# Kernel tuning notes

Hardware: AMD Instinct MI355X
Metric: run time of the kernel (lower is better)

## Reference

```python
import jax, jax.numpy as jnp
import numpy as np

NUM_RELATIONS = 16


def rgcn_conv(x, src, dst, etype, W, root, b):
    """PyG-style RGCNConv: per-relation mean aggregation + root weight + bias.

    x: [N, din]; W: [R, din, dout]; root: [din, dout]; b: [dout].
    """
    N, din = x.shape
    R = W.shape[0]
    E = src.shape[0]
    xe = x[src]                                   # [E, din] gather
    seg = etype * N + dst                          # combined (relation, dst) key
    sums = jax.ops.segment_sum(xe, seg, num_segments=R * N)        # [R*N, din]
    cnt = jax.ops.segment_sum(jnp.ones((E,), x.dtype), seg, num_segments=R * N)
    mean = (sums / jnp.maximum(cnt, 1.0)[:, None]).reshape(R, N, din)
    # mean-then-transform == PyG transform-then-mean (linearity)
    out = jnp.einsum('rnd,rde->ne', mean, W) + x @ root + b
    return out


def setup_inputs() -> dict:
    key = jax.random.key(0)
    ks = jax.random.split(key, 8)
    N, E, DIN, H, OUT, R = 40000, 640000, 386, 256, 2, NUM_RELATIONS
    x = jax.random.normal(ks[0], (N, DIN), dtype=jnp.float32)
    edge_index = jax.random.randint(ks[1], (2, E), 0, N, dtype=jnp.int64)
    edge_type = jax.random.randint(ks[2], (E,), 0, R, dtype=jnp.int64)
    s1 = 1.0 / np.sqrt(DIN)
    s2 = 1.0 / np.sqrt(H)
    W1 = jax.random.normal(ks[3], (R, DIN, H), dtype=jnp.float32) * s1
    root1 = jax.random.normal(ks[4], (DIN, H), dtype=jnp.float32) * s1
    b1 = jnp.zeros((H,), dtype=jnp.float32)
    W2 = jax.random.normal(ks[5], (R, H, OUT), dtype=jnp.float32) * s2
    root2 = jax.random.normal(ks[6], (H, OUT), dtype=jnp.float32) * s2
    b2 = jnp.zeros((OUT,), dtype=jnp.float32)
    return {"x": x, "edge_index": edge_index, "edge_type": edge_type,
            "W1": W1, "root1": root1, "b1": b1,
            "W2": W2, "root2": root2, "b2": b2}


def reference(x, edge_index, edge_type, W1, root1, b1, W2, root2, b2):
    src, dst = edge_index[0], edge_index[1]
    h = jax.nn.relu(rgcn_conv(x, src, dst, edge_type, W1, root1, b1))
    h = rgcn_conv(h, src, dst, edge_type, W2, root2, b2)
    return jnp.tanh(h)
```

## Files before the change

kernel.cpp:

```cpp
#include <hip/hip_runtime.h>
#include <cstdint>
#include <cstddef>

#define N_NODES 40000
#define DIN     386
#define H1      256
#define NREL    16
#define KPAD    416
#define MPAD    40064
#define NBREL   16
#define NCOL1   ((NREL + 1) * H1)
#define Y2C     (2 * NREL + 2)
#define N2PAD   48
#define LDB2    264
#define NWPR    625
#define ROWCAP  26112
#define NMTCP   208

typedef __attribute__((ext_vector_type(8))) short s8v;
typedef __attribute__((ext_vector_type(4))) float f4v;

__device__ __forceinline__ uint16_t f2h(float f) {
  _Float16 h = (_Float16)f;
  return *(uint16_t*)&h;
}
__device__ __forceinline__ float h2f(uint16_t u) {
  _Float16 h = *(_Float16*)&u;
  return (float)h;
}
__device__ __forceinline__ f4v mfma_f16(s8v a, s8v b, f4v c) {
  asm("v_mfma_f32_16x16x32_f16 %0, %1, %2, %0" : "+v"(c) : "v"(a), "v"(b));
  return c;
}
__device__ __forceinline__ void gload16(const uint16_t* g, const uint16_t* lds) {
  __builtin_amdgcn_global_load_lds(
      (const __attribute__((address_space(1))) unsigned int*)g,
      (__attribute__((address_space(3))) unsigned int*)lds, 16, 0, 0);
}

__global__ void k_count(const int* __restrict__ src, const int* __restrict__ dst,
                        const int* __restrict__ et, int* __restrict__ deg,
                        uint8_t* __restrict__ flagS, int* __restrict__ epos, int E) {
  int e = blockIdx.x * 256 + threadIdx.x;
  if (e < E) {
    epos[e] = atomicAdd(&deg[dst[e]], 1);
    flagS[et[e] * N_NODES + src[e]] = 1;
  }
}

__global__ void k_wcount(const uint8_t* __restrict__ flagS, int* __restrict__ wcnt) {
  int i = blockIdx.x * 256 + threadIdx.x;
  unsigned long long m = __ballot(flagS[i] != 0);
  if ((threadIdx.x & 63) == 0) wcnt[i >> 6] = (int)__popcll(m);
}

__global__ void k_wscan(const int* __restrict__ wcnt, int* __restrict__ wbase,
                        int* __restrict__ nsrc) {
  __shared__ int sd[1024];
  int r = blockIdx.x, t = threadIdx.x;
  int v = (t < NWPR) ? wcnt[r * NWPR + t] : 0;
  sd[t] = v;
  __syncthreads();
  for (int off = 1; off < 1024; off <<= 1) {
    int x = (t >= off) ? sd[t - off] : 0;
    __syncthreads();
    sd[t] += x;
    __syncthreads();
  }
  if (t < NWPR) wbase[r * NWPR + t] = sd[t] - v;
  if (t == NWPR - 1) nsrc[r] = sd[t];
}

__global__ void k_assign(const uint8_t* __restrict__ flagS,
                         const int* __restrict__ wbase,
                         int* __restrict__ posmap, int* __restrict__ srclist) {
  int i = blockIdx.x * 256 + threadIdx.x;
  int lane = threadIdx.x & 63;
  bool act = flagS[i] != 0;
  unsigned long long m = __ballot(act);
  if (act) {
    int pre = (int)__popcll(m & ((1ULL << lane) - 1));
    int p = wbase[i >> 6] + pre;
    int r = i / N_NODES, s = i - r * N_NODES;
    if (p < ROWCAP) {
      posmap[i] = p;
      srclist[r * ROWCAP + p] = s;
    } else {
      posmap[i] = ROWCAP - 1;
    }
  }
}

__global__ void k_s1(const int* __restrict__ deg, int* __restrict__ rowptr,
                     int* __restrict__ bsum) {
  __shared__ int sd[1024];
  int t = threadIdx.x;
  int i = blockIdx.x * 1024 + t;
  int v = (i < N_NODES) ? deg[i] : 0;
  sd[t] = v;
  __syncthreads();
  for (int off = 1; off < 1024; off <<= 1) {
    int x = (t >= off) ? sd[t - off] : 0;
    __syncthreads();
    sd[t] += x;
    __syncthreads();
  }
  if (i < N_NODES) rowptr[i + 1] = sd[t];
  if (t == 1023) bsum[blockIdx.x] = sd[t];
}
__global__ void k_s2(const int* __restrict__ bsum, int* __restrict__ bscan,
                     int* __restrict__ rowptr, int nb) {
  int lane = threadIdx.x & 63;
  int own = (lane < nb) ? bsum[lane] : 0;
  int v = own;
  for (int off = 1; off < 64; off <<= 1) {
    int x = __shfl_up(v, off);
    if (lane >= off) v += x;
  }
  if (lane < nb) bscan[lane] = v - own;
  if (lane == 0) rowptr[0] = 0;
}
__global__ void k_s3(const int* __restrict__ bscan, int* __restrict__ rowptr) {
  int i = blockIdx.x * 1024 + threadIdx.x;
  if (i < N_NODES && blockIdx.x > 0) rowptr[i + 1] += bscan[blockIdx.x];
}

__global__ void k_scatter(const int* __restrict__ src, const int* __restrict__ dst,
                          const int* __restrict__ et, const int* __restrict__ rowptr,
                          const int* __restrict__ epos, const int* __restrict__ posmap,
                          int* __restrict__ e_rp, int* __restrict__ e_rs, int E) {
  int e = blockIdx.x * 256 + threadIdx.x;
  if (e < E) {
    int d = dst[e], r = et[e], s = src[e];
    int idx = rowptr[d] + epos[e];
    e_rp[idx] = (r << 16) | posmap[r * N_NODES + s];
    e_rs[idx] = (r << 16) | s;
  }
}

__global__ void k_pack_x(const float* __restrict__ x, uint16_t* __restrict__ xh) {
  long long i = (long long)blockIdx.x * 256 + threadIdx.x;
  if (i >= (long long)MPAD * (KPAD / 8)) return;
  int n = (int)(i / (KPAD / 8)), kv = (int)(i % (KPAD / 8));
  int k = kv * 8;
  uint4 o = {0u, 0u, 0u, 0u};
  if (n < N_NODES) {
    const float* xr = x + (long long)n * DIN;
    if (k + 8 <= DIN) {
      float2 p0 = *(const float2*)(xr + k);
      float2 p1 = *(const float2*)(xr + k + 2);
      float2 p2 = *(const float2*)(xr + k + 4);
      float2 p3 = *(const float2*)(xr + k + 6);
      o.x = (uint32_t)f2h(p0.x) | ((uint32_t)f2h(p0.y) << 16);
      o.y = (uint32_t)f2h(p1.x) | ((uint32_t)f2h(p1.y) << 16);
      o.z = (uint32_t)f2h(p2.x) | ((uint32_t)f2h(p2.y) << 16);
      o.w = (uint32_t)f2h(p3.x) | ((uint32_t)f2h(p3.y) << 16);
    } else if (k < DIN) {
      uint16_t t[8];
#pragma unroll
      for (int j = 0; j < 8; ++j) t[j] = (k + j < DIN) ? f2h(xr[k + j]) : 0;
      o.x = (uint32_t)t[0] | ((uint32_t)t[1] << 16);
      o.y = (uint32_t)t[2] | ((uint32_t)t[3] << 16);
      o.z = (uint32_t)t[4] | ((uint32_t)t[5] << 16);
      o.w = (uint32_t)t[6] | ((uint32_t)t[7] << 16);
    }
  }
  *(uint4*)(xh + (long long)n * KPAD + k) = o;
}

__global__ void k_pack_b1(const float* __restrict__ W1, const float* __restrict__ root1,
                          uint16_t* __restrict__ Bh) {
  long long i = (long long)blockIdx.x * 256 + threadIdx.x;
  if (i >= (long long)NCOL1 * KPAD) return;
  int c = (int)(i / KPAD), k = (int)(i % KPAD);
  float v = 0.0f;
  if (k < DIN) {
    if (c < NREL * H1) {
      int r = c >> 8, j = c & 255;
      v = W1[((long long)r * DIN + k) * H1 + j];
    } else {
      v = root1[(long long)k * H1 + (c - NREL * H1)];
    }
  }
  Bh[i] = f2h(v);
}

__global__ void k_pack_b2(const float* __restrict__ W2, const float* __restrict__ root2,
                          uint16_t* __restrict__ b2h) {
  int i = blockIdx.x * 256 + threadIdx.x;
  if (i >= N2PAD * H1) return;
  int c = i >> 8, k = i & 255;
  float v = 0.0f;
  if (c < 2 * NREL) { int r = c >> 1, j = c & 1; v = W2[(r * H1 + k) * 2 + j]; }
  else if (c < Y2C) v = root2[k * 2 + (c - 2 * NREL)];
  b2h[i] = f2h(v);
}

__global__ __launch_bounds__(256) void k_gemm1(
    const uint16_t* __restrict__ A, const uint16_t* __restrict__ B,
    uint16_t* __restrict__ C, int ldc, int nb,
    const int* __restrict__ srclist, const int* __restrict__ nsrc, int r0) {
  __shared__ __align__(16) uint16_t sA[2][128 * 32];
  __shared__ __align__(16) uint16_t sB[2][256 * 32];
  int tid = threadIdx.x;
  int lane = tid & 63, w = tid >> 6;
  int wr = w >> 1, wcn = w & 1;

  int f = blockIdx.x;
  int xcd = f & 7, j = f >> 3;
  int yt = j % nb, mtj = j / nb;
  int mt = mtj * 8 + xcd;
  int rel = r0 + yt;
  int ns = nsrc[rel];
  if (ns > ROWCAP) ns = ROWCAP;
  long long bm = (long long)mt * 128;
  if (bm >= ns) return;
  long long bn = (long long)yt * 256;

  int lrow = lane & 15;
  int lko = (((lane >> 4) ^ ((lane >> 1) & 3)) * 8);

  int arow = tid >> 2;
  int skel = (((tid & 3) ^ ((tid >> 3) & 3)) * 8);

  const int* sl = srclist + rel * ROWCAP;
  int ia = (int)bm + arow;
  int ib = ia + 64;
  long long rowA0 = sl[ia < ns ? ia : 0];
  long long rowA1 = sl[ib < ns ? ib : 0];

  const uint16_t* gA0 = A + rowA0 * KPAD + skel;
  const uint16_t* gA1 = A + rowA1 * KPAD + skel;
  const uint16_t* gB0 = B + (bn + arow) * KPAD + skel;
  const uint16_t* gB1 = gB0 + (long long)64 * KPAD;
  const uint16_t* gB2 = gB0 + (long long)128 * KPAD;
  const uint16_t* gB3 = gB0 + (long long)192 * KPAD;

  f4v zero = {0.f, 0.f, 0.f, 0.f};
  f4v acc[4][8];
#pragma unroll
  for (int i = 0; i < 4; ++i)
#pragma unroll
    for (int jj = 0; jj < 8; ++jj) acc[i][jj] = zero;

  gload16(gA0, sA[0] + w * 512);
  gload16(gA1, sA[0] + 2048 + w * 512);
  gload16(gB0, sB[0] + w * 512);
  gload16(gB1, sB[0] + 2048 + w * 512);
  gload16(gB2, sB[0] + 4096 + w * 512);
  gload16(gB3, sB[0] + 6144 + w * 512);

  const int NIT = KPAD / 32;
  int cur = 0;
  for (int it = 0; it < NIT; ++it) {
    if (it + 1 < NIT) {
      int kk = (it + 1) * 32;
      int nxt = cur ^ 1;
      gload16(gA0 + kk, sA[nxt] + w * 512);
      gload16(gA1 + kk, sA[nxt] + 2048 + w * 512);
      gload16(gB0 + kk, sB[nxt] + w * 512);
      gload16(gB1 + kk, sB[nxt] + 2048 + w * 512);
      gload16(gB2 + kk, sB[nxt] + 4096 + w * 512);
      gload16(gB3 + kk, sB[nxt] + 6144 + w * 512);
      asm volatile("s_waitcnt vmcnt(6)" ::: "memory");
    } else {
      asm volatile("s_waitcnt vmcnt(0)" ::: "memory");
    }
    __builtin_amdgcn_s_barrier();

    const uint16_t* pA = sA[cur];
    const uint16_t* pB = sB[cur];
    s8v af[4];
#pragma unroll
    for (int mi = 0; mi < 4; ++mi)
      af[mi] = *(const s8v*)(pA + (wr * 64 + mi * 16 + lrow) * 32 + lko);
#pragma unroll
    for (int ni = 0; ni < 8; ++ni) {
      s8v bf = *(const s8v*)(pB + (wcn * 128 + ni * 16 + lrow) * 32 + lko);
#pragma unroll
      for (int mi = 0; mi < 4; ++mi)
        acc[mi][ni] = mfma_f16(af[mi], bf, acc[mi][ni]);
    }
    __builtin_amdgcn_s_barrier();
    cur ^= 1;
  }

  int rg = (lane >> 4) * 4;
#pragma unroll
  for (int mi = 0; mi < 4; ++mi) {
#pragma unroll
    for (int ni = 0; ni < 8; ++ni) {
      long long col = bn + wcn * 128 + ni * 16 + (lane & 15);
#pragma unroll
      for (int r2 = 0; r2 < 4; ++r2) {
        long long row = bm + wr * 64 + mi * 16 + rg + r2;
        C[row * ldc + col] = f2h(acc[mi][ni][r2]);
      }
    }
  }
}

__global__ __launch_bounds__(512) void k_gemmroot(
    const uint16_t* __restrict__ A, const uint16_t* __restrict__ B,
    uint16_t* __restrict__ h) {
  __shared__ __align__(16) uint16_t sA[2][128 * 32];
  __shared__ __align__(16) uint16_t sB[2][256 * 32];
  int tid = threadIdx.x;
  int lane = tid & 63, w = tid >> 6;
  int wr = w >> 2, wc = w & 3;
  long long bm = (long long)blockIdx.x * 128;

  int lrow = lane & 15;
  int lko = (((lane >> 4) ^ ((lane >> 1) & 3)) * 8);
  int arow = tid >> 2;
  int skel = (((tid & 3) ^ ((tid >> 3) & 3)) * 8);

  const uint16_t* gA  = A + (bm + arow) * KPAD + skel;
  const uint16_t* gB0 = B + arow * KPAD + skel;
  const uint16_t* gB1 = B + (arow + 128) * KPAD + skel;

  f4v zero = {0.f, 0.f, 0.f, 0.f};
  f4v acc[4][4];
#pragma unroll
  for (int i = 0; i < 4; ++i)
#pragma unroll
    for (int j = 0; j < 4; ++j) acc[i][j] = zero;

  gload16(gA, sA[0] + w * 512);
  gload16(gB0, sB[0] + w * 512);
  gload16(gB1, sB[0] + 4096 + w * 512);

  const int NIT = KPAD / 32;
  int cur = 0;
  for (int it = 0; it < NIT; ++it) {
    if (it + 1 < NIT) {
      int kk = (it + 1) * 32;
      int nxt = cur ^ 1;
      gload16(gA + kk, sA[nxt] + w * 512);
      gload16(gB0 + kk, sB[nxt] + w * 512);
      gload16(gB1 + kk, sB[nxt] + 4096 + w * 512);
      asm volatile("s_waitcnt vmcnt(3)" ::: "memory");
    } else {
      asm volatile("s_waitcnt vmcnt(0)" ::: "memory");
    }
    __builtin_amdgcn_s_barrier();

    const uint16_t* pA = sA[cur];
    const uint16_t* pB = sB[cur];
    s8v af[4];
#pragma unroll
    for (int mi = 0; mi < 4; ++mi)
      af[mi] = *(const s8v*)(pA + (wr * 64 + mi * 16 + lrow) * 32 + lko);
#pragma unroll
    for (int ni = 0; ni < 4; ++ni) {
      s8v bf = *(const s8v*)(pB + (wc * 64 + ni * 16 + lrow) * 32 + lko);
#pragma unroll
      for (int mi = 0; mi < 4; ++mi)
        acc[mi][ni] = mfma_f16(af[mi], bf, acc[mi][ni]);
    }
    __builtin_amdgcn_s_barrier();
    cur ^= 1;
  }

  int rg = (lane >> 4) * 4;
#pragma unroll
  for (int mi = 0; mi < 4; ++mi) {
#pragma unroll
    for (int ni = 0; ni < 4; ++ni) {
      int col = wc * 64 + ni * 16 + (lane & 15);
#pragma unroll
      for (int r2 = 0; r2 < 4; ++r2) {
        long long row = bm + wr * 64 + mi * 16 + rg + r2;
        if (row < N_NODES) h[row * H1 + col] = f2h(acc[mi][ni][r2]);
      }
    }
  }
}

__global__ __launch_bounds__(256) void k_agg1(
    const uint16_t* __restrict__ y1,
    const int* __restrict__ e_rp, const int* __restrict__ rowptr,
    uint16_t* __restrict__ h, const float* __restrict__ b1,
    int r0, int nb, int ldy, int fin) {
  int n = blockIdx.x * 4 + (threadIdx.x >> 6);
  int lane = threadIdx.x & 63;
  if (n >= N_NODES) return;
  int e0 = rowptr[n], e1 = rowptr[n + 1];
  int deg = e1 - e0;

  int mrp = (lane < deg) ? e_rp[e0 + lane] : -1;
  int myrel = mrp >> 16;
  int cmine = 0;
#pragma unroll
  for (int r = 0; r < 16; ++r) {
    unsigned long long m = __ballot(myrel == r);
    if (lane == r) cmine = (int)__popcll(m);
  }
  for (int base = e0 + 64; base < e1; base += 64) {
    int vv = (base + lane < e1) ? e_rp[base + lane] : -1;
    int rr = vv >> 16;
#pragma unroll
    for (int r = 0; r < 16; ++r) {
      unsigned long long m = __ballot(rr == r);
      if (lane == r) cmine += (int)__popcll(m);
    }
  }

  float4 acc = {0.f, 0.f, 0.f, 0.f};
  int dcap = deg <= 64 ? deg : 64;
  for (int j = 0; j < dcap; ++j) {
    int v = __shfl(mrp, j);
    int rel = v >> 16;
    int off = rel - r0;
    int cv = __shfl(cmine, rel & 15);
    if ((unsigned)off < (unsigned)nb) {
      int pos = v & 0xFFFF;
      float w = 1.0f / (float)cv;
      uint2 q = *(const uint2*)(y1 + (long long)pos * ldy + off * H1 + lane * 4);
      acc.x += w * h2f((uint16_t)q.x);
      acc.y += w * h2f((uint16_t)(q.x >> 16));
      acc.z += w * h2f((uint16_t)q.y);
      acc.w += w * h2f((uint16_t)(q.y >> 16));
    }
  }
  for (int e = e0 + 64; e < e1; ++e) {
    int v = e_rp[e];
    int rel = v >> 16;
    int off = rel - r0;
    int cv = __shfl(cmine, rel & 15);
    if ((unsigned)off < (unsigned)nb) {
      int pos = v & 0xFFFF;
      float w = 1.0f / (float)cv;
      uint2 q = *(const uint2*)(y1 + (long long)pos * ldy + off * H1 + lane * 4);
      acc.x += w * h2f((uint16_t)q.x);
      acc.y += w * h2f((uint16_t)(q.x >> 16));
      acc.z += w * h2f((uint16_t)q.y);
      acc.w += w * h2f((uint16_t)(q.y >> 16));
    }
  }

  uint16_t* hp = h + (long long)n * H1 + lane * 4;
  uint2 hv = *(const uint2*)hp;
  float o0 = h2f((uint16_t)hv.x) + acc.x;
  float o1 = h2f((uint16_t)(hv.x >> 16)) + acc.y;
  float o2 = h2f((uint16_t)hv.y) + acc.z;
  float o3 = h2f((uint16_t)(hv.y >> 16)) + acc.w;
  if (fin) {
    float4 bv = *(const float4*)(b1 + lane * 4);
    o0 += bv.x; o0 = o0 > 0.f ? o0 : 0.f;
    o1 += bv.y; o1 = o1 > 0.f ? o1 : 0.f;
    o2 += bv.z; o2 = o2 > 0.f ? o2 : 0.f;
    o3 += bv.w; o3 = o3 > 0.f ? o3 : 0.f;
  }
  uint2 o;
  o.x = (uint32_t)f2h(o0) | ((uint32_t)f2h(o1) << 16);
  o.y = (uint32_t)f2h(o2) | ((uint32_t)f2h(o3) << 16);
  *(uint2*)hp = o;
}

__global__ __launch_bounds__(256) void k_gemm2m(
    const uint16_t* __restrict__ h, const uint16_t* __restrict__ b2h,
    uint16_t* __restrict__ y2) {
  __shared__ __align__(16) uint16_t sB[N2PAD * LDB2];
  __shared__ __align__(16) uint16_t sA[128 * 32];
  int tid = threadIdx.x, lane = tid & 63, w = tid >> 6;
  long long bm = (long long)blockIdx.x * 128;

  for (int cid = tid; cid < N2PAD * 32; cid += 256) {
    int row = cid >> 5, off = cid & 31;
    *(uint4*)(&sB[row * LDB2 + off * 8]) = *(const uint4*)(b2h + row * H1 + off * 8);
  }

  f4v zero = {0.f, 0.f, 0.f, 0.f};
  f4v acc[2][3];
#pragma unroll
  for (int i = 0; i < 2; ++i)
#pragma unroll
    for (int j = 0; j < 3; ++j) acc[i][j] = zero;

  int lrow = lane & 15;
  int lko = (((lane >> 4) ^ ((lane >> 1) & 3)) * 8);
  int srow0 = w * 32 + (lane >> 2), srow1 = srow0 + 16;
  int skel = (((lane & 3) ^ ((lane >> 3) & 3)) * 8);

  for (int kk = 0; kk < H1; kk += 32) {
    gload16(h + (bm + srow0) * H1 + kk + skel, sA + w * 1024);
    gload16(h + (bm + srow1) * H1 + kk + skel, sA + w * 1024 + 512);
    __syncthreads();

    s8v ah[2];
#pragma unroll
    for (int mi = 0; mi < 2; ++mi)
      ah[mi] = *(const s8v*)(sA + (w * 32 + mi * 16 + lrow) * 32 + lko);
#pragma unroll
    for (int nj = 0; nj < 3; ++nj) {
      s8v bh = *(const s8v*)(&sB[(nj * 16 + lrow) * LDB2 + kk + ((lane >> 4) * 8)]);
#pragma unroll
      for (int mi = 0; mi < 2; ++mi)
        acc[mi][nj] = mfma_f16(ah[mi], bh, acc[mi][nj]);
    }
    __syncthreads();
  }
  int rg = (lane >> 4) * 4;
#pragma unroll
  for (int mi = 0; mi < 2; ++mi) {
#pragma unroll
    for (int nj = 0; nj < 3; ++nj) {
      int col = nj * 16 + (lane & 15);
      if (col < Y2C) {
#pragma unroll
        for (int r2 = 0; r2 < 4; ++r2) {
          long long row = bm + w * 32 + mi * 16 + rg + r2;
          if (row < N_NODES) y2[row * Y2C + col] = f2h(acc[mi][nj][r2]);
        }
      }
    }
  }
}

__global__ void k_agg2(const uint16_t* __restrict__ y2, const int* __restrict__ e_rs,
                       const int* __restrict__ rowptr, const float* __restrict__ b2,
                       float* __restrict__ out) {
  int n = blockIdx.x * 4 + (threadIdx.x >> 6);
  int lane = threadIdx.x & 63;
  if (n >= N_NODES) return;
  int e0 = rowptr[n], e1 = rowptr[n + 1];

  int v0 = (e0 + lane < e1) ? e_rs[e0 + lane] : -1;
  int rel0 = v0 >> 16;
  int cmine = 0;
#pragma unroll
  for (int r = 0; r < 16; ++r) {
    unsigned long long m = __ballot(rel0 == r);
    if (lane == r) cmine = (int)__popcll(m);
  }
  for (int base = e0 + 64; base < e1; base += 64) {
    int vv = (base + lane < e1) ? e_rs[base + lane] : -1;
    int rr = vv >> 16;
#pragma unroll
    for (int r = 0; r < 16; ++r) {
      unsigned long long m = __ballot(rr == r);
      if (lane == r) cmine += (int)__popcll(m);
    }
  }

  float a0 = 0.f, a1 = 0.f;
  {
    int cv = __shfl(cmine, rel0 & 15);
    if (v0 >= 0) {
      int s = v0 & 0xFFFF;
      float w = 1.0f / (float)cv;
      uint32_t q = *(const uint32_t*)(y2 + (long long)s * Y2C + rel0 * 2);
      a0 += w * h2f((uint16_t)q);
      a1 += w * h2f((uint16_t)(q >> 16));
    }
  }
  for (int base = e0 + 64; base < e1; base += 64) {
    int vv = (base + lane < e1) ? e_rs[base + lane] : -1;
    int rr = vv >> 16;
    int cv = __shfl(cmine, rr & 15);
    if (vv >= 0) {
      int s = vv & 0xFFFF;
      float w = 1.0f / (float)cv;
      uint32_t q = *(const uint32_t*)(y2 + (long long)s * Y2C + rr * 2);
      a0 += w * h2f((uint16_t)q);
      a1 += w * h2f((uint16_t)(q >> 16));
    }
  }
#pragma unroll
  for (int off = 32; off > 0; off >>= 1) {
    a0 += __shfl_down(a0, off);
    a1 += __shfl_down(a1, off);
  }
  if (lane == 0) {
    uint32_t q = *(const uint32_t*)(y2 + (long long)n * Y2C + 2 * NREL);
    a0 += h2f((uint16_t)q) + b2[0];
    a1 += h2f((uint16_t)(q >> 16)) + b2[1];
    out[n * 2] = tanhf(a0);
    out[n * 2 + 1] = tanhf(a1);
  }
}

extern "C" void kernel_launch(void* const* d_in, const int* in_sizes, int n_in,
                              void* d_out, int out_size, void* d_ws, size_t ws_size,
                              hipStream_t stream) {
  const float* x     = (const float*)d_in[0];
  const int*   ei    = (const int*)d_in[1];
  const int*   et    = (const int*)d_in[2];
  const float* W1    = (const float*)d_in[3];
  const float* root1 = (const float*)d_in[4];
  const float* b1    = (const float*)d_in[5];
  const float* W2    = (const float*)d_in[6];
  const float* root2 = (const float*)d_in[7];
  const float* b2    = (const float*)d_in[8];
  const int E = in_sizes[2];
  const int* src = ei;
  const int* dst = ei + E;

  char* ws = (char*)d_ws;
  size_t off = 0;
  auto alloc = [&](size_t bytes) {
    size_t o = off; off += (bytes + 255) & ~(size_t)255; return o;
  };
  size_t o_deg  = alloc((size_t)(N_NODES + 1) * 4);
  size_t o_flag = alloc((size_t)NREL * N_NODES);
  size_t zero_bytes = off;
  size_t o_nsrc = alloc(64 * 4);
  size_t o_wcnt = alloc((size_t)NREL * NWPR * 4);
  size_t o_wbas = alloc((size_t)NREL * NWPR * 4);
  size_t o_h    = alloc((size_t)MPAD * H1 * 2);
  size_t o_rp   = alloc((size_t)(N_NODES + 1) * 4);
  size_t o_bsum = alloc(64 * 4);
  size_t o_bscn = alloc(64 * 4);
  size_t o_erp  = alloc((size_t)E * 4);
  size_t o_ers  = alloc((size_t)E * 4);
  size_t o_slst = alloc((size_t)NREL * ROWCAP * 4);
  size_t o_xh   = alloc((size_t)MPAD * KPAD * 2);
  size_t o_b1h  = alloc((size_t)NCOL1 * KPAD * 2);
  size_t o_b2h  = alloc((size_t)N2PAD * H1 * 2);
  size_t o_y2   = alloc((size_t)N_NODES * Y2C * 2);
  size_t o_y1   = off;

  int*      deg  = (int*)(ws + o_deg);
  uint8_t*  flg  = (uint8_t*)(ws + o_flag);
  int*      nsrc = (int*)(ws + o_nsrc);
  int*      wcnt = (int*)(ws + o_wcnt);
  int*      wbas = (int*)(ws + o_wbas);
  uint16_t* h    = (uint16_t*)(ws + o_h);
  int*      rp   = (int*)(ws + o_rp);
  int*      bsum = (int*)(ws + o_bsum);
  int*      bscn = (int*)(ws + o_bscn);
  int*      erp  = (int*)(ws + o_erp);
  int*      ers  = (int*)(ws + o_ers);
  int*      slst = (int*)(ws + o_slst);
  uint16_t* xh   = (uint16_t*)(ws + o_xh);
  uint16_t* b1h  = (uint16_t*)(ws + o_b1h);
  uint16_t* b2h  = (uint16_t*)(ws + o_b2h);
  uint16_t* y2   = (uint16_t*)(ws + o_y2);
  uint16_t* y1   = (uint16_t*)(ws + o_y1);
  int*      epin = (int*)(ws + o_y1);
  int*      pmap = (int*)(ws + o_y1 + (((size_t)E * 4 + 255) & ~(size_t)255));

  size_t per_block = (size_t)ROWCAP * H1 * 2;
  int G = 1;
  if (ws_size > o_y1 + per_block) {
    size_t g = (ws_size - o_y1) / per_block;
    G = (int)(g > (size_t)NBREL ? (size_t)NBREL : g);
  }
  int npass = (NBREL + G - 1) / G;
  int Gb = (NBREL + npass - 1) / npass;

  const int NSB = (N_NODES + 1023) / 1024;
  const int NCB = NREL * N_NODES / 256;

  hipMemsetAsync(ws, 0, zero_bytes, stream);
  k_count<<<(E + 255) / 256, 256, 0, stream>>>(src, dst, et, deg, flg, epin, E);
  k_wcount<<<NCB, 256, 0, stream>>>(flg, wcnt);
  k_wscan<<<NREL, 1024, 0, stream>>>(wcnt, wbas, nsrc);
  k_assign<<<NCB, 256, 0, stream>>>(flg, wbas, pmap, slst);
  k_s1<<<NSB, 1024, 0, stream>>>(deg, rp, bsum);
  k_s2<<<1, 64, 0, stream>>>(bsum, bscn, rp, NSB);
  k_s3<<<NSB, 1024, 0, stream>>>(bscn, rp);
  k_scatter<<<(E + 255) / 256, 256, 0, stream>>>(src, dst, et, rp, epin, pmap,
                                                 erp, ers, E);
  k_pack_x<<<(unsigned)(((long long)MPAD * (KPAD / 8) + 255) / 256), 256, 0, stream>>>(x, xh);
  k_pack_b1<<<(unsigned)(((long long)NCOL1 * KPAD + 255) / 256), 256, 0, stream>>>(W1, root1, b1h);
  k_pack_b2<<<(N2PAD * H1 + 255) / 256, 256, 0, stream>>>(W2, root2, b2h);

  k_gemmroot<<<MPAD / 128, 512, 0, stream>>>(xh, b1h + (size_t)NREL * H1 * KPAD, h);

  int r0 = 0;
  for (int p = 0; p < npass; ++p) {
    int nb = (NBREL - r0 < Gb) ? (NBREL - r0) : Gb;
    int nwg = NMTCP * nb;
    k_gemm1<<<nwg, 256, 0, stream>>>(xh, b1h + (size_t)r0 * H1 * KPAD, y1, nb * H1,
                                     nb, slst, nsrc, r0);
    k_agg1<<<(N_NODES + 3) / 4, 256, 0, stream>>>(y1, erp, rp, h, b1,
                                                  r0, nb, nb * H1,
                                                  (p == npass - 1) ? 1 : 0);
    r0 += nb;
  }
  k_gemm2m<<<MPAD / 128, 256, 0, stream>>>(h, b2h, y2);
  k_agg2<<<(N_NODES + 3) / 4, 256, 0, stream>>>(y2, ers, rp, b2,
                                                (float*)d_out);
  (void)n_in; (void)out_size;
}
```

Baseline: 384.1 us.

## Merge preprocessing launches and fold root GEMM into relation GEMM grid

The relation-word scan and degree block scan are merged into one launch, the three-step scan collapses to two by recomputing the block offsets inside k_s3, and the three pack kernels become one. The separate root GEMM kernel is removed; its tiles are appended as extra workgroups to the first-pass relation GEMM so they share one launch and can fill idle CUs. This cuts launch count and serialization, at the cost of the root tiles now using the 256-thread 128x256 tile configuration instead of the dedicated 512-thread kernel.

```diff
diff --git a/kernel.cpp b/kernel.cpp
--- a/kernel.cpp
+++ b/kernel.cpp
@@ -8,6 +8,7 @@
 #define NREL    16
 #define KPAD    416
 #define MPAD    40064
+#define NMT     313
 #define NBREL   16
 #define NCOL1   ((NREL + 1) * H1)
 #define Y2C     (2 * NREL + 2)
@@ -16,6 +17,10 @@
 #define NWPR    625
 #define ROWCAP  26112
 #define NMTCP   208
+#define NSB     40
+#define NXB     8138
+#define NB1B    7072
+#define NB2B    48
 
 typedef __attribute__((ext_vector_type(8))) short s8v;
 typedef __attribute__((ext_vector_type(4))) float f4v;
@@ -54,21 +59,39 @@
   if ((threadIdx.x & 63) == 0) wcnt[i >> 6] = (int)__popcll(m);
 }
 
-__global__ void k_wscan(const int* __restrict__ wcnt, int* __restrict__ wbase,
-                        int* __restrict__ nsrc) {
+__global__ void k_scan1(const int* __restrict__ wcnt, int* __restrict__ wbase,
+                        int* __restrict__ nsrc, const int* __restrict__ deg,
+                        int* __restrict__ rowptr, int* __restrict__ bsum) {
   __shared__ int sd[1024];
-  int r = blockIdx.x, t = threadIdx.x;
-  int v = (t < NWPR) ? wcnt[r * NWPR + t] : 0;
-  sd[t] = v;
-  __syncthreads();
-  for (int off = 1; off < 1024; off <<= 1) {
-    int x = (t >= off) ? sd[t - off] : 0;
+  int t = threadIdx.x;
+  if (blockIdx.x < NREL) {
+    int r = blockIdx.x;
+    int v = (t < NWPR) ? wcnt[r * NWPR + t] : 0;
+    sd[t] = v;
     __syncthreads();
-    sd[t] += x;
+    for (int off = 1; off < 1024; off <<= 1) {
+      int x = (t >= off) ? sd[t - off] : 0;
+      __syncthreads();
+      sd[t] += x;
+      __syncthreads();
+    }
+    if (t < NWPR) wbase[r * NWPR + t] = sd[t] - v;
+    if (t == NWPR - 1) nsrc[r] = sd[t];
+  } else {
+    int b = blockIdx.x - NREL;
+    int i = b * 1024 + t;
+    int v = (i < N_NODES) ? deg[i] : 0;
+    sd[t] = v;
     __syncthreads();
-  }
-  if (t < NWPR) wbase[r * NWPR + t] = sd[t] - v;
-  if (t == NWPR - 1) nsrc[r] = sd[t];
+    for (int off = 1; off < 1024; off <<= 1) {
+      int x = (t >= off) ? sd[t - off] : 0;
+      __syncthreads();
+      sd[t] += x;
+      __syncthreads();
+    }
+    if (i < N_NODES) rowptr[i + 1] = sd[t];
+    if (t == 1023) bsum[b] = sd[t];
+  }
 }
 
 __global__ void k_assign(const uint8_t* __restrict__ flagS,
@@ -91,38 +114,24 @@
   }
 }
 
-__global__ void k_s1(const int* __restrict__ deg, int* __restrict__ rowptr,
-                     int* __restrict__ bsum) {
-  __shared__ int sd[1024];
-  int t = threadIdx.x;
-  int i = blockIdx.x * 1024 + t;
-  int v = (i < N_NODES) ? deg[i] : 0;
-  sd[t] = v;
+__global__ void k_s3(const int* __restrict__ bsum, int* __restrict__ rowptr) {
+  __shared__ int s_off;
+  int b = blockIdx.x, t = threadIdx.x;
+  if (t < 64) {
+    int lane = t;
+    int v = (lane < NSB) ? bsum[lane] : 0;
+    for (int o = 1; o < 64; o <<= 1) {
+      int x = __shfl_up(v, o);
+      if (lane >= o) v += x;
+    }
+    int off = (b == 0) ? 0 : __shfl(v, b - 1);
+    if (lane == 0) s_off = off;
+  }
   __syncthreads();
-  for (int off = 1; off < 1024; off <<= 1) {
-    int x = (t >= off) ? sd[t - off] : 0;
-    __syncthreads();
-    sd[t] += x;
-    __syncthreads();
-  }
-  if (i < N_NODES) rowptr[i + 1] = sd[t];
-  if (t == 1023) bsum[blockIdx.x] = sd[t];
-}
-__global__ void k_s2(const int* __restrict__ bsum, int* __restrict__ bscan,
-                     int* __restrict__ rowptr, int nb) {
-  int lane = threadIdx.x & 63;
-  int own = (lane < nb) ? bsum[lane] : 0;
-  int v = own;
-  for (int off = 1; off < 64; off <<= 1) {
-    int x = __shfl_up(v, off);
-    if (lane >= off) v += x;
-  }
-  if (lane < nb) bscan[lane] = v - own;
-  if (lane == 0) rowptr[0] = 0;
-}
-__global__ void k_s3(const int* __restrict__ bscan, int* __restrict__ rowptr) {
-  int i = blockIdx.x * 1024 + threadIdx.x;
-  if (i < N_NODES && blockIdx.x > 0) rowptr[i + 1] += bscan[blockIdx.x];
+  int off = s_off;
+  int i = b * 1024 + t;
+  if (i < N_NODES && b > 0) rowptr[i + 1] += off;
+  if (b == 0 && t == 0) rowptr[0] = 0;
 }
 
 __global__ void k_scatter(const int* __restrict__ src, const int* __restrict__ dst,
@@ -138,67 +147,67 @@
   }
 }
 
-__global__ void k_pack_x(const float* __restrict__ x, uint16_t* __restrict__ xh) {
-  long long i = (long long)blockIdx.x * 256 + threadIdx.x;
-  if (i >= (long long)MPAD * (KPAD / 8)) return;
-  int n = (int)(i / (KPAD / 8)), kv = (int)(i % (KPAD / 8));
-  int k = kv * 8;
-  uint4 o = {0u, 0u, 0u, 0u};
-  if (n < N_NODES) {
-    const float* xr = x + (long long)n * DIN;
-    if (k + 8 <= DIN) {
-      float2 p0 = *(const float2*)(xr + k);
-      float2 p1 = *(const float2*)(xr + k + 2);
-      float2 p2 = *(const float2*)(xr + k + 4);
-      float2 p3 = *(const float2*)(xr + k + 6);
-      o.x = (uint32_t)f2h(p0.x) | ((uint32_t)f2h(p0.y) << 16);
-      o.y = (uint32_t)f2h(p1.x) | ((uint32_t)f2h(p1.y) << 16);
-      o.z = (uint32_t)f2h(p2.x) | ((uint32_t)f2h(p2.y) << 16);
-      o.w = (uint32_t)f2h(p3.x) | ((uint32_t)f2h(p3.y) << 16);
-    } else if (k < DIN) {
-      uint16_t t[8];
-#pragma unroll
-      for (int j = 0; j < 8; ++j) t[j] = (k + j < DIN) ? f2h(xr[k + j]) : 0;
-      o.x = (uint32_t)t[0] | ((uint32_t)t[1] << 16);
-      o.y = (uint32_t)t[2] | ((uint32_t)t[3] << 16);
-      o.z = (uint32_t)t[4] | ((uint32_t)t[5] << 16);
-      o.w = (uint32_t)t[6] | ((uint32_t)t[7] << 16);
-    }
-  }
-  *(uint4*)(xh + (long long)n * KPAD + k) = o;
-}
-
-__global__ void k_pack_b1(const float* __restrict__ W1, const float* __restrict__ root1,
-                          uint16_t* __restrict__ Bh) {
-  long long i = (long long)blockIdx.x * 256 + threadIdx.x;
-  if (i >= (long long)NCOL1 * KPAD) return;
-  int c = (int)(i / KPAD), k = (int)(i % KPAD);
-  float v = 0.0f;
-  if (k < DIN) {
-    if (c < NREL * H1) {
-      int r = c >> 8, j = c & 255;
-      v = W1[((long long)r * DIN + k) * H1 + j];
-    } else {
-      v = root1[(long long)k * H1 + (c - NREL * H1)];
-    }
-  }
-  Bh[i] = f2h(v);
-}
-
-__global__ void k_pack_b2(const float* __restrict__ W2, const float* __restrict__ root2,
-                          uint16_t* __restrict__ b2h) {
-  int i = blockIdx.x * 256 + threadIdx.x;
-  if (i >= N2PAD * H1) return;
-  int c = i >> 8, k = i & 255;
-  float v = 0.0f;
-  if (c < 2 * NREL) { int r = c >> 1, j = c & 1; v = W2[(r * H1 + k) * 2 + j]; }
-  else if (c < Y2C) v = root2[k * 2 + (c - 2 * NREL)];
-  b2h[i] = f2h(v);
+__global__ void k_pack(const float* __restrict__ x, const float* __restrict__ W1,
+                       const float* __restrict__ root1, const float* __restrict__ W2,
+                       const float* __restrict__ root2, uint16_t* __restrict__ xh,
+                       uint16_t* __restrict__ b1h, uint16_t* __restrict__ b2h) {
+  int bb = blockIdx.x;
+  int tid = threadIdx.x;
+  if (bb < NXB) {
+    long long i = (long long)bb * 256 + tid;
+    if (i >= (long long)MPAD * (KPAD / 8)) return;
+    int n = (int)(i / (KPAD / 8)), kv = (int)(i % (KPAD / 8));
+    int k = kv * 8;
+    uint4 o = {0u, 0u, 0u, 0u};
+    if (n < N_NODES) {
+      const float* xr = x + (long long)n * DIN;
+      if (k + 8 <= DIN) {
+        float2 p0 = *(const float2*)(xr + k);
+        float2 p1 = *(const float2*)(xr + k + 2);
+        float2 p2 = *(const float2*)(xr + k + 4);
+        float2 p3 = *(const float2*)(xr + k + 6);
+        o.x = (uint32_t)f2h(p0.x) | ((uint32_t)f2h(p0.y) << 16);
+        o.y = (uint32_t)f2h(p1.x) | ((uint32_t)f2h(p1.y) << 16);
+        o.z = (uint32_t)f2h(p2.x) | ((uint32_t)f2h(p2.y) << 16);
+        o.w = (uint32_t)f2h(p3.x) | ((uint32_t)f2h(p3.y) << 16);
+      } else if (k < DIN) {
+        uint16_t t[8];
+#pragma unroll
+        for (int j = 0; j < 8; ++j) t[j] = (k + j < DIN) ? f2h(xr[k + j]) : 0;
+        o.x = (uint32_t)t[0] | ((uint32_t)t[1] << 16);
+        o.y = (uint32_t)t[2] | ((uint32_t)t[3] << 16);
+        o.z = (uint32_t)t[4] | ((uint32_t)t[5] << 16);
+        o.w = (uint32_t)t[6] | ((uint32_t)t[7] << 16);
+      }
+    }
+    *(uint4*)(xh + (long long)n * KPAD + k) = o;
+  } else if (bb < NXB + NB1B) {
+    long long i = (long long)(bb - NXB) * 256 + tid;
+    int c = (int)(i / KPAD), k = (int)(i % KPAD);
+    float v = 0.0f;
+    if (k < DIN) {
+      if (c < NREL * H1) {
+        int r = c >> 8, j = c & 255;
+        v = W1[((long long)r * DIN + k) * H1 + j];
+      } else {
+        v = root1[(long long)k * H1 + (c - NREL * H1)];
+      }
+    }
+    b1h[i] = f2h(v);
+  } else {
+    int i = (bb - NXB - NB1B) * 256 + tid;
+    int c = i >> 8, k = i & 255;
+    float v = 0.0f;
+    if (c < 2 * NREL) { int r = c >> 1, j = c & 1; v = W2[(r * H1 + k) * 2 + j]; }
+    else if (c < Y2C) v = root2[k * 2 + (c - 2 * NREL)];
+    b2h[i] = f2h(v);
+  }
 }
 
 __global__ __launch_bounds__(256) void k_gemm1(
     const uint16_t* __restrict__ A, const uint16_t* __restrict__ B,
-    uint16_t* __restrict__ C, int ldc, int nb,
+    const uint16_t* __restrict__ Broot, uint16_t* __restrict__ C,
+    uint16_t* __restrict__ h, int ldc, int nb, int jrel,
     const int* __restrict__ srclist, const int* __restrict__ nsrc, int r0) {
   __shared__ __align__(16) uint16_t sA[2][128 * 32];
   __shared__ __align__(16) uint16_t sB[2][256 * 32];
@@ -208,14 +217,25 @@
 
   int f = blockIdx.x;
   int xcd = f & 7, j = f >> 3;
-  int yt = j % nb, mtj = j / nb;
-  int mt = mtj * 8 + xcd;
-  int rel = r0 + yt;
-  int ns = nsrc[rel];
-  if (ns > ROWCAP) ns = ROWCAP;
+  bool root = (j >= jrel);
+  int mt, yt = 0, ns;
+  const uint16_t* Bp;
+  long long bn = 0;
+  if (!root) {
+    yt = j % nb;
+    mt = (j / nb) * 8 + xcd;
+    ns = nsrc[r0 + yt];
+    if (ns > ROWCAP) ns = ROWCAP;
+    Bp = B;
+    bn = (long long)yt * 256;
+  } else {
+    mt = (j - jrel) * 8 + xcd;
+    if (mt >= NMT) return;
+    ns = N_NODES;
+    Bp = Broot;
+  }
   long long bm = (long long)mt * 128;
   if (bm >= ns) return;
-  long long bn = (long long)yt * 256;
 
   int lrow = lane & 15;
   int lko = (((lane >> 4) ^ ((lane >> 1) & 3)) * 8);
@@ -223,15 +243,20 @@
   int arow = tid >> 2;
   int skel = (((tid & 3) ^ ((tid >> 3) & 3)) * 8);
 
-  const int* sl = srclist + rel * ROWCAP;
-  int ia = (int)bm + arow;
-  int ib = ia + 64;
-  long long rowA0 = sl[ia < ns ? ia : 0];
-  long long rowA1 = sl[ib < ns ? ib : 0];
+  long long rowA0, rowA1;
+  if (!root) {
+    const int* sl = srclist + (r0 + yt) * ROWCAP;
+    int ia = (int)bm + arow, ib = ia + 64;
+    rowA0 = sl[ia < ns ? ia : 0];
+    rowA1 = sl[ib < ns ? ib : 0];
+  } else {
+    rowA0 = bm + arow;
+    rowA1 = bm + arow + 64;
+  }
 
   const uint16_t* gA0 = A + rowA0 * KPAD + skel;
   const uint16_t* gA1 = A + rowA1 * KPAD + skel;
-  const uint16_t* gB0 = B + (bn + arow) * KPAD + skel;
+  const uint16_t* gB0 = Bp + (bn + arow) * KPAD + skel;
   const uint16_t* gB1 = gB0 + (long long)64 * KPAD;
   const uint16_t* gB2 = gB0 + (long long)128 * KPAD;
   const uint16_t* gB3 = gB0 + (long long)192 * KPAD;
@@ -286,102 +311,39 @@
   }
 
   int rg = (lane >> 4) * 4;
-#pragma unroll
-  for (int mi = 0; mi < 4; ++mi) {
-#pragma unroll
-    for (int ni = 0; ni < 8; ++ni) {
-      long long col = bn + wcn * 128 + ni * 16 + (lane & 15);
-#pragma unroll
-      for (int r2 = 0; r2 < 4; ++r2) {
-        long long row = bm + wr * 64 + mi * 16 + rg + r2;
-        C[row * ldc + col] = f2h(acc[mi][ni][r2]);
+  if (!root) {
+#pragma unroll
+    for (int mi = 0; mi < 4; ++mi) {
+#pragma unroll
+      for (int ni = 0; ni < 8; ++ni) {
+        long long col = bn + wcn * 128 + ni * 16 + (lane & 15);
+#pragma unroll
+        for (int r2 = 0; r2 < 4; ++r2) {
+          long long row = bm + wr * 64 + mi * 16 + rg + r2;
+          C[row * ldc + col] = f2h(acc[mi][ni][r2]);
+        }
       }
     }
-  }
-}
-
-__global__ __launch_bounds__(512) void k_gemmroot(
-    const uint16_t* __restrict__ A, const uint16_t* __restrict__ B,
-    uint16_t* __restrict__ h) {
-  __shared__ __align__(16) uint16_t sA[2][128 * 32];
-  __shared__ __align__(16) uint16_t sB[2][256 * 32];
-  int tid = threadIdx.x;
-  int lane = tid & 63, w = tid >> 6;
-  int wr = w >> 2, wc = w & 3;
-  long long bm = (long long)blockIdx.x * 128;
-
-  int lrow = lane & 15;
-  int lko = (((lane >> 4) ^ ((lane >> 1) & 3)) * 8);
-  int arow = tid >> 2;
-  int skel = (((tid & 3) ^ ((tid >> 3) & 3)) * 8);
-
-  const uint16_t* gA  = A + (bm + arow) * KPAD + skel;
-  const uint16_t* gB0 = B + arow * KPAD + skel;
-  const uint16_t* gB1 = B + (arow + 128) * KPAD + skel;
-
-  f4v zero = {0.f, 0.f, 0.f, 0.f};
-  f4v acc[4][4];
-#pragma unroll
-  for (int i = 0; i < 4; ++i)
-#pragma unroll
-    for (int j = 0; j < 4; ++j) acc[i][j] = zero;
-
-  gload16(gA, sA[0] + w * 512);
-  gload16(gB0, sB[0] + w * 512);
-  gload16(gB1, sB[0] + 4096 + w * 512);
-
-  const int NIT = KPAD / 32;
-  int cur = 0;
-  for (int it = 0; it < NIT; ++it) {
-    if (it + 1 < NIT) {
-      int kk = (it + 1) * 32;
-      int nxt = cur ^ 1;
-      gload16(gA + kk, sA[nxt] + w * 512);
-      gload16(gB0 + kk, sB[nxt] + w * 512);
-      gload16(gB1 + kk, sB[nxt] + 4096 + w * 512);
-      asm volatile("s_waitcnt vmcnt(3)" ::: "memory");
-    } else {
-      asm volatile("s_waitcnt vmcnt(0)" ::: "memory");
-    }
-    __builtin_amdgcn_s_barrier();
-
-    const uint16_t* pA = sA[cur];
-    const uint16_t* pB = sB[cur];
-    s8v af[4];
-#pragma unroll
-    for (int mi = 0; mi < 4; ++mi)
-      af[mi] = *(const s8v*)(pA + (wr * 64 + mi * 16 + lrow) * 32 + lko);
-#pragma unroll
-    for (int ni = 0; ni < 4; ++ni) {
-      s8v bf = *(const s8v*)(pB + (wc * 64 + ni * 16 + lrow) * 32 + lko);
-#pragma unroll
-      for (int mi = 0; mi < 4; ++mi)
-        acc[mi][ni] = mfma_f16(af[mi], bf, acc[mi][ni]);
-    }
-    __builtin_amdgcn_s_barrier();
-    cur ^= 1;
-  }
-
-  int rg = (lane >> 4) * 4;
-#pragma unroll
-  for (int mi = 0; mi < 4; ++mi) {
-#pragma unroll
-    for (int ni = 0; ni < 4; ++ni) {
-      int col = wc * 64 + ni * 16 + (lane & 15);
-#pragma unroll
-      for (int r2 = 0; r2 < 4; ++r2) {
-        long long row = bm + wr * 64 + mi * 16 + rg + r2;
-        if (row < N_NODES) h[row * H1 + col] = f2h(acc[mi][ni][r2]);
+  } else {
+#pragma unroll
+    for (int mi = 0; mi < 4; ++mi) {
+#pragma unroll
+      for (int ni = 0; ni < 8; ++ni) {
+        int col = wcn * 128 + ni * 16 + (lane & 15);
+#pragma unroll
+        for (int r2 = 0; r2 < 4; ++r2) {
+          long long row = bm + wr * 64 + mi * 16 + rg + r2;
+          if (row < N_NODES) h[row * H1 + col] = f2h(acc[mi][ni][r2]);
+        }
       }
     }
   }
 }
 
 __global__ __launch_bounds__(256) void k_agg1(
-    const uint16_t* __restrict__ y1,
-    const int* __restrict__ e_rp, const int* __restrict__ rowptr,
-    uint16_t* __restrict__ h, const float* __restrict__ b1,
-    int r0, int nb, int ldy, int fin) {
+    const uint16_t* __restrict__ y1, const int* __restrict__ e_rp,
+    const int* __restrict__ rowptr, uint16_t* __restrict__ h,
+    const float* __restrict__ b1, int r0, int nb, int ldy, int fin) {
   int n = blockIdx.x * 4 + (threadIdx.x >> 6);
   int lane = threadIdx.x & 63;
   if (n >= N_NODES) return;
@@ -611,7 +573,6 @@
   size_t o_h    = alloc((size_t)MPAD * H1 * 2);
   size_t o_rp   = alloc((size_t)(N_NODES + 1) * 4);
   size_t o_bsum = alloc(64 * 4);
-  size_t o_bscn = alloc(64 * 4);
   size_t o_erp  = alloc((size_t)E * 4);
   size_t o_ers  = alloc((size_t)E * 4);
   size_t o_slst = alloc((size_t)NREL * ROWCAP * 4);
@@ -629,7 +590,6 @@
   uint16_t* h    = (uint16_t*)(ws + o_h);
   int*      rp   = (int*)(ws + o_rp);
   int*      bsum = (int*)(ws + o_bsum);
-  int*      bscn = (int*)(ws + o_bscn);
   int*      erp  = (int*)(ws + o_erp);
   int*      ers  = (int*)(ws + o_ers);
   int*      slst = (int*)(ws + o_slst);
@@ -650,31 +610,29 @@
   int npass = (NBREL + G - 1) / G;
   int Gb = (NBREL + npass - 1) / npass;
 
-  const int NSB = (N_NODES + 1023) / 1024;
   const int NCB = NREL * N_NODES / 256;
+  const int JROOT = 40;
 
   hipMemsetAsync(ws, 0, zero_bytes, stream);
   k_count<<<(E + 255) / 256, 256, 0, stream>>>(src, dst, et, deg, flg, epin, E);
   k_wcount<<<NCB, 256, 0, stream>>>(flg, wcnt);
-  k_wscan<<<NREL, 1024, 0, stream>>>(wcnt, wbas, nsrc);
+  k_scan1<<<NREL + NSB, 1024, 0, stream>>>(wcnt, wbas, nsrc, deg, rp, bsum);
   k_assign<<<NCB, 256, 0, stream>>>(flg, wbas, pmap, slst);
-  k_s1<<<NSB, 1024, 0, stream>>>(deg, rp, bsum);
-  k_s2<<<1, 64, 0, stream>>>(bsum, bscn, rp, NSB);
-  k_s3<<<NSB, 1024, 0, stream>>>(bscn, rp);
+  k_s3<<<NSB, 1024, 0, stream>>>(bsum, rp);
   k_scatter<<<(E + 255) / 256, 256, 0, stream>>>(src, dst, et, rp, epin, pmap,
                                                  erp, ers, E);
-  k_pack_x<<<(unsigned)(((long long)MPAD * (KPAD / 8) + 255) / 256), 256, 0, stream>>>(x, xh);
-  k_pack_b1<<<(unsigned)(((long long)NCOL1 * KPAD + 255) / 256), 256, 0, stream>>>(W1, root1, b1h);
-  k_pack_b2<<<(N2PAD * H1 + 255) / 256, 256, 0, stream>>>(W2, root2, b2h);
-
-  k_gemmroot<<<MPAD / 128, 512, 0, stream>>>(xh, b1h + (size_t)NREL * H1 * KPAD, h);
+  k_pack<<<NXB + NB1B + NB2B, 256, 0, stream>>>(x, W1, root1, W2, root2,
+                                                xh, b1h, b2h);
 
   int r0 = 0;
   for (int p = 0; p < npass; ++p) {
     int nb = (NBREL - r0 < Gb) ? (NBREL - r0) : Gb;
-    int nwg = NMTCP * nb;
-    k_gemm1<<<nwg, 256, 0, stream>>>(xh, b1h + (size_t)r0 * H1 * KPAD, y1, nb * H1,
-                                     nb, slst, nsrc, r0);
+    int jrel = (NMTCP / 8) * nb;
+    int jroot = (p == 0) ? JROOT : 0;
+    int nwg = 8 * (jrel + jroot);
+    k_gemm1<<<nwg, 256, 0, stream>>>(xh, b1h + (size_t)r0 * H1 * KPAD,
+                                     b1h + (size_t)NREL * H1 * KPAD, y1, h,
+                                     nb * H1, nb, jrel, slst, nsrc, r0);
     k_agg1<<<(N_NODES + 3) / 4, 256, 0, stream>>>(y1, erp, rp, h, b1,
                                                   r0, nb, nb * H1,
                                                   (p == npass - 1) ? 1 : 0);
```

Result: faster. 362.0 us (-5.8%).
